# Kernel tuning notes

Hardware: AMD Instinct MI355X
Metric: run time of the kernel (lower is better)

Reference implementation:

```python
import jax, jax.numpy as jnp
import numpy as np
from jax import lax

B, N, C = 8, 8192, 64
ODR, K, OUT = 4, 32, 128
S = N // ODR
EPS = 1e-5


def _lbr(h, W, b, g, be):
    # h: [M, K, Cin] -> linear -> BN (training-mode batch stats over (M,K) per channel) -> relu
    y = jnp.einsum('mki,oi->mko', h, W) + b
    mean = y.mean(axis=(0, 1))
    var = ((y - mean) ** 2).mean(axis=(0, 1))  # biased var, as torch BN uses for normalization
    y = (y - mean) * lax.rsqrt(var + EPS) * g + be
    return jax.nn.relu(y)


def setup_inputs() -> dict:
    key = jax.random.key(0)
    ks = jax.random.split(key, 12)
    x = jax.random.normal(ks[0], (B, N, C), dtype=jnp.float32)
    coor = jax.random.normal(ks[1], (B, N, 3), dtype=jnp.float32)
    indx = jax.random.permutation(ks[2], N)[:S]  # like torch.randperm(N)[:S]
    w1 = jax.random.normal(ks[3], (OUT, 2 * C), dtype=jnp.float32) * (2 * C) ** -0.5
    b1 = jax.random.normal(ks[4], (OUT,), dtype=jnp.float32) * 0.01
    g1 = jax.random.uniform(ks[5], (OUT,), dtype=jnp.float32, minval=0.5, maxval=1.5)
    be1 = jax.random.normal(ks[6], (OUT,), dtype=jnp.float32) * 0.01
    w2 = jax.random.normal(ks[7], (OUT, OUT), dtype=jnp.float32) * OUT ** -0.5
    b2 = jax.random.normal(ks[8], (OUT,), dtype=jnp.float32) * 0.01
    g2 = jax.random.uniform(ks[9], (OUT,), dtype=jnp.float32, minval=0.5, maxval=1.5)
    be2 = jax.random.normal(ks[10], (OUT,), dtype=jnp.float32) * 0.01
    return dict(x=x, coor=coor, indx=indx, w1=w1, b1=b1, g1=g1, be1=be1,
                w2=w2, b2=b2, g2=g2, be2=be2)


def reference(x, coor, indx, w1, b1, g1, be1, w2, b2, g2, be2):
    sampled_coor = coor[:, indx, :]  # [B,S,3]
    sampled_x = x[:, indx, :]        # [B,S,C]
    # pairwise squared distances [B,S,N]
    dist = jnp.sum((coor[:, None, :, :] - sampled_coor[:, :, None, :]) ** 2, axis=-1)
    # k smallest distances == argsort(dist)[..., :K]
    _, knn_idx = lax.top_k(-dist, K)  # [B,S,K]
    knn_x = jax.vmap(lambda xb, ib: xb[ib])(x, knn_idx)  # [B,S,K,C]
    rep_x = jnp.broadcast_to(sampled_x[:, :, None, :], (x.shape[0], S, K, x.shape[2]))
    feat = jnp.concatenate([rep_x, knn_x - rep_x], axis=-1)  # [B,S,K,2C]
    feat = feat.reshape(x.shape[0] * S, K, 2 * x.shape[2])
    h = _lbr(feat, w1, b1, g1, be1)
    h = _lbr(h, w2, b2, g2, be2)
    h = h.reshape(x.shape[0], S, K, -1)
    out = jnp.max(h, axis=2)  # [B,S,OUT]
    return out, sampled_coor
```

## Files before the change

kernel.cpp:

```cpp
#include <hip/hip_runtime.h>
#include <stdint.h>


#define N_    8192
#define GPB_  8

typedef __attribute__((ext_vector_type(8))) short bf8;
typedef __attribute__((ext_vector_type(16))) float f32x16;
typedef __attribute__((ext_vector_type(2))) float f32x2;

__device__ __forceinline__ unsigned int bf1u(float f) {
  unsigned int u = __float_as_uint(f);
  return (u + 0x7fffu + ((u >> 16) & 1u)) >> 16;
}
__device__ __forceinline__ unsigned int bfpair(float lo, float hi) {
  return bf1u(lo) | (bf1u(hi) << 16);
}

__device__ __forceinline__ f32x2 pk_add(f32x2 a, f32x2 b) {
  f32x2 d;
  asm("v_pk_add_f32 %0, %1, %2" : "=v"(d) : "v"(a), "v"(b));
  return d;
}
__device__ __forceinline__ f32x2 pk_mul(f32x2 a, f32x2 b) {
  f32x2 d;
  asm("v_pk_mul_f32 %0, %1, %2" : "=v"(d) : "v"(a), "v"(b));
  return d;
}

__global__ __launch_bounds__(256) void kprep(const float* __restrict__ w1,
                                             const float* __restrict__ w2,
                                             const float* __restrict__ coor,
                                             const int* __restrict__ indx,
                                             unsigned short* __restrict__ w1b,
                                             unsigned short* __restrict__ w2b,
                                             float* __restrict__ outc,
                                             float* __restrict__ soa) {
  int e = blockIdx.x * 256 + threadIdx.x;
  if (e < 16384) {
    w1b[e] = (unsigned short)bf1u(w1[e]);
  } else if (e < 32768) {
    int e2 = e - 16384;
    w2b[e2] = (unsigned short)bf1u(w2[e2]);
  } else if (e < 81920) {
    int e2 = e - 32768;
    int bs = e2 / 3, c = e2 - bs * 3;
    int b = bs >> 11, s = bs & 2047;
    outc[e2] = coor[(b * N_ + indx[s]) * 3 + c];
  } else {
    int p = e - 81920;
    const int b = p >> 13, i = p & 8191;
    const float* src = coor + (size_t)p * 3;
    float* dst = soa + b * 24576;
    dst[i]         = src[0];
    dst[8192 + i]  = src[1];
    dst[16384 + i] = src[2];
  }
}

__global__ __launch_bounds__(256, 8) void kknn(const float* __restrict__ soa,
                                               const int* __restrict__ indx,
                                               int* __restrict__ knn) {
  __shared__ __align__(16) float4 sdist4[4 * 256];
  __shared__ float smin[128];
  __shared__ float smrg[64];
  __shared__ float sT;
  __shared__ unsigned long long cands[128];
  __shared__ unsigned long long ssort[128];
  __shared__ int ccnt;

  const int gid = blockIdx.x;
  const int b = gid >> 11, s = gid & 2047;
  const int tid = threadIdx.x;
  const int w = tid >> 6, lane = tid & 63;
  const float* Xb = soa + b * 24576;
  const float* Yb = Xb + 8192;
  const float* Zb = Xb + 16384;
  const int qi = indx[s];
  const float qx = Xb[qi], qy = Yb[qi], qz = Zb[qi];
  const f32x2 nqx = {-qx, -qx}, nqy = {-qy, -qy}, nqz = {-qz, -qz};

  f32x2 rd[8];
  f32x2 dmL = {3.4e38f, 3.4e38f}, dmH = {3.4e38f, 3.4e38f};
#pragma unroll
  for (int it = 0; it < 8; ++it) {
    const int ofs = (it << 10) + (tid << 2);
    union { float4 f4; f32x2 h[2]; } X, Y, Z;
    X.f4 = *(const float4*)(Xb + ofs);
    Y.f4 = *(const float4*)(Yb + ofs);
    Z.f4 = *(const float4*)(Zb + ofs);
    const f32x2 dxl = pk_add(X.h[0], nqx), dyl = pk_add(Y.h[0], nqy),
                dzl = pk_add(Z.h[0], nqz);
    const f32x2 dxh = pk_add(X.h[1], nqx), dyh = pk_add(Y.h[1], nqy),
                dzh = pk_add(Z.h[1], nqz);
    const f32x2 sl =
        pk_add(pk_add(pk_mul(dxl, dxl), pk_mul(dyl, dyl)), pk_mul(dzl, dzl));
    const f32x2 sh =
        pk_add(pk_add(pk_mul(dxh, dxh), pk_mul(dyh, dyh)), pk_mul(dzh, dzh));
    dmL.x = fminf(dmL.x, sl.x);
    dmL.y = fminf(dmL.y, sl.y);
    dmH.x = fminf(dmH.x, sh.x);
    dmH.y = fminf(dmH.y, sh.y);
    if (it < 4) {
      rd[it * 2] = sl;
      rd[it * 2 + 1] = sh;
    } else {
      union { float4 f4; f32x2 h[2]; } st;
      st.h[0] = sl;
      st.h[1] = sh;
      sdist4[((it - 4) << 8) + tid] = st.f4;
    }
  }
  float dmin = fminf(fminf(dmL.x, dmL.y), fminf(dmH.x, dmH.y));
  if (tid == 0) ccnt = 0;
  if (tid < 128) cands[tid] = ~0ULL;

  float v = dmin;
#pragma unroll
  for (int k = 2; k <= 64; k <<= 1) {
#pragma unroll
    for (int j = k >> 1; j >= 1; j >>= 1) {
      const float o = __shfl_xor(v, j, 64);
      const bool dirAsc = ((lane & k) == 0);
      const bool lower = ((lane & j) == 0);
      const float lo = fminf(v, o), hi = fmaxf(v, o);
      v = (dirAsc == lower) ? lo : hi;
    }
  }
  if (lane < 32) smin[w * 32 + lane] = v;
  __syncthreads();
  if (w < 2) {
    float a = (lane < 32) ? smin[w * 64 + lane] : smin[w * 64 + 32 + (63 - lane)];
#pragma unroll
    for (int j = 32; j >= 1; j >>= 1) {
      const float o = __shfl_xor(a, j, 64);
      const float lo = fminf(a, o), hi = fmaxf(a, o);
      a = ((lane & j) == 0) ? lo : hi;
    }
    if (lane < 32) smrg[w * 32 + lane] = a;
  }
  __syncthreads();
  if (w == 0) {
    float a = (lane < 32) ? smrg[lane] : smrg[32 + (63 - lane)];
#pragma unroll
    for (int j = 32; j >= 1; j >>= 1) {
      const float o = __shfl_xor(a, j, 64);
      const float lo = fminf(a, o), hi = fmaxf(a, o);
      a = ((lane & j) == 0) ? lo : hi;
    }
    if (lane == 31) sT = a;
  }
  __syncthreads();
  const float T = sT;

#pragma unroll
  for (int t = 0; t < 8; ++t) {
    const int p0 = ((t >> 1) << 10) + (tid << 2) + ((t & 1) << 1);
    const float d0 = rd[t].x, d1 = rd[t].y;
    if (d0 <= T) {
      const int pos = atomicAdd(&ccnt, 1);
      if (pos < 128)
        cands[pos] = ((unsigned long long)__float_as_uint(d0) << 32) |
                     (unsigned int)p0;
    }
    if (d1 <= T) {
      const int pos = atomicAdd(&ccnt, 1);
      if (pos < 128)
        cands[pos] = ((unsigned long long)__float_as_uint(d1) << 32) |
                     (unsigned int)(p0 + 1);
    }
  }
#pragma unroll
  for (int it = 4; it < 8; ++it) {
    const float4 d4 = sdist4[((it - 4) << 8) + tid];
    const int p0 = (it << 10) + (tid << 2);
    const float dd[4] = {d4.x, d4.y, d4.z, d4.w};
#pragma unroll
    for (int j = 0; j < 4; ++j) {
      if (dd[j] <= T) {
        const int pos = atomicAdd(&ccnt, 1);
        if (pos < 128)
          cands[pos] = ((unsigned long long)__float_as_uint(dd[j]) << 32) |
                       (unsigned int)(p0 + j);
      }
    }
  }
  __syncthreads();

  if (w < 2) {
    unsigned long long kv = cands[w * 64 + lane];
#pragma unroll
    for (int k = 2; k <= 64; k <<= 1) {
#pragma unroll
      for (int j = k >> 1; j >= 1; j >>= 1) {
        const unsigned long long o = __shfl_xor(kv, j, 64);
        const bool dirAsc = ((lane & k) == 0);
        const bool lower = ((lane & j) == 0);
        const unsigned long long lo = o < kv ? o : kv;
        const unsigned long long hi = o < kv ? kv : o;
        kv = (dirAsc == lower) ? lo : hi;
      }
    }
    ssort[w * 64 + lane] = kv;
  }
  __syncthreads();
  if (w == 0) {
    const unsigned long long a = ssort[lane];
    const unsigned long long b2 = ssort[64 + 63 - lane];
    unsigned long long m = a < b2 ? a : b2;
#pragma unroll
    for (int j = 32; j >= 1; j >>= 1) {
      const unsigned long long o = __shfl_xor(m, j, 64);
      const unsigned long long lo = o < m ? o : m;
      const unsigned long long hi = o < m ? m : o;
      m = ((lane & j) == 0) ? lo : hi;
    }
    if (lane < 32) knn[gid * 32 + lane] = (int)(unsigned int)m;
  }
}

template <int PHASE>
__global__ __launch_bounds__(256, 4) void kphase(
    const float* __restrict__ x, const int* __restrict__ indx,
    const int* __restrict__ knn, const float* __restrict__ b1,
    const unsigned short* __restrict__ w1b, const unsigned short* __restrict__ w2b,
    const float* __restrict__ b2, const float* __restrict__ st1,
    float* __restrict__ part, float* __restrict__ mout) {
  __shared__ __align__(16) float sx[64];
  __shared__ __align__(16) unsigned short sxb[72];
  __shared__ __align__(16) unsigned short dls[32 * 68 + 8];
  __shared__ __align__(16) unsigned short h1[PHASE == 2 ? 32 * 136 : 8];

  const int tid = threadIdx.x;
  const int w = tid >> 6;
  const int lane = tid & 63;
  const int m = lane & 31, q2 = lane >> 5;
  const int col = (w << 5) + m;
  const int r8 = tid >> 3, c8 = (tid & 7) * 8;

  const int bb = blockIdx.x & 7;
  const int jj = blockIdx.x >> 3;
  const float* xb = x + (size_t)bb * (N_ * 64);
  const int gidbase = (bb << 11) + jj * GPB_;

  bf8 bf1[8];
#pragma unroll
  for (int t = 0; t < 8; ++t)
    bf1[t] = *(const bf8*)&w1b[col * 128 + t * 16 + q2 * 8];
  bf8 bf2[8];
  float s1 = 0.f, t1 = 0.f, b2v = 0.f;
  if constexpr (PHASE == 2) {
#pragma unroll
    for (int t = 0; t < 8; ++t)
      bf2[t] = *(const bf8*)&w2b[col * 128 + t * 16 + q2 * 8];
    s1 = st1[col];
    t1 = st1[128 + col];
    b2v = b2[col];
  }
  (void)w2b; (void)b2; (void)st1; (void)mout;
  const float b1c = b1[col];

  float sum = 0.f, ssq = 0.f;

  int idxp = indx[jj * GPB_];
  float sxv = (tid < 64) ? xb[(size_t)idxp * 64 + tid] : 0.f;
  int nbr = knn[(size_t)gidbase * 32 + r8];

#pragma unroll 1
  for (int g = 0; g < GPB_; ++g) {
    const int gid = gidbase + g;
    if (tid < 64) sx[tid] = sxv;
    __syncthreads();

    {
      const float* xrow = xb + (size_t)nbr * 64 + c8;
      const float4 xa = *(const float4*)(xrow);
      const float4 xc = *(const float4*)(xrow + 4);
      const float4 sa = *(const float4*)(sx + c8);
      const float4 sc = *(const float4*)(sx + c8 + 4);
      uint2 lo, hi;
      lo.x = bfpair(xa.x - sa.x, xa.y - sa.y);
      lo.y = bfpair(xa.z - sa.z, xa.w - sa.w);
      hi.x = bfpair(xc.x - sc.x, xc.y - sc.y);
      hi.y = bfpair(xc.z - sc.z, xc.w - sc.w);
      *(uint2*)&dls[r8 * 68 + c8] = lo;
      *(uint2*)&dls[r8 * 68 + c8 + 4] = hi;
    }
    if (tid < 16) {
      const float4 sv = *(const float4*)(sx + tid * 4);
      uint2 p;
      p.x = bfpair(sv.x, sv.y);
      p.y = bfpair(sv.z, sv.w);
      *(uint2*)&sxb[tid * 4] = p;
    }

    if (g + 1 < GPB_) {
      const int s1n = jj * GPB_ + g + 1;
      const int idx1 = indx[s1n];
      sxv = (tid < 64) ? xb[(size_t)idx1 * 64 + tid] : 0.f;
      nbr = knn[(size_t)(gid + 1) * 32 + r8];
    }
    __syncthreads();

    bf8 af[8];
#pragma unroll
    for (int t = 0; t < 4; ++t) {
      union { bf8 v; uint2 u[2]; } fa;
      fa.u[0] = *(const uint2*)&sxb[t * 16 + q2 * 8];
      fa.u[1] = *(const uint2*)&sxb[t * 16 + q2 * 8 + 4];
      af[t] = fa.v;
    }
#pragma unroll
    for (int t = 0; t < 4; ++t) {
      union { bf8 v; uint2 u[2]; } fa;
      fa.u[0] = *(const uint2*)&dls[m * 68 + t * 16 + q2 * 8];
      fa.u[1] = *(const uint2*)&dls[m * 68 + t * 16 + q2 * 8 + 4];
      af[4 + t] = fa.v;
    }

    f32x16 acc;
#pragma unroll
    for (int r = 0; r < 16; ++r) acc[r] = b1c;
#pragma unroll
    for (int t = 0; t < 8; ++t)
      acc = __builtin_amdgcn_mfma_f32_32x32x16_bf16(af[t], bf1[t], acc, 0, 0, 0);

    if constexpr (PHASE == 1) {
#pragma unroll
      for (int r = 0; r < 16; ++r) {
        const float v = acc[r];
        sum += v;
        ssq = fmaf(v, v, ssq);
      }
    } else {
#pragma unroll
      for (int r = 0; r < 16; ++r) {
        const float hv = fmaxf(0.f, fmaf(acc[r], s1, t1));
        const int row = (r & 3) + ((r >> 2) << 3) + (q2 << 2);
        h1[row * 136 + col] = (unsigned short)bf1u(hv);
      }
      __syncthreads();

      f32x16 acc2;
#pragma unroll
      for (int r = 0; r < 16; ++r) acc2[r] = b2v;
#pragma unroll
      for (int t = 0; t < 8; ++t) {
        const bf8 a2 = *(const bf8*)&h1[m * 136 + t * 16 + q2 * 8];
        acc2 = __builtin_amdgcn_mfma_f32_32x32x16_bf16(a2, bf2[t], acc2, 0, 0, 0);
      }

      float mx = -1e30f;
#pragma unroll
      for (int r = 0; r < 16; ++r) {
        const float v = acc2[r];
        sum += v;
        ssq = fmaf(v, v, ssq);
        mx = fmaxf(mx, v);
      }
      mx = fmaxf(mx, __shfl_xor(mx, 32, 64));
      if (lane < 32) mout[(size_t)gid * 128 + col] = mx;
    }
  }

  sum += __shfl_xor(sum, 32, 64);
  ssq += __shfl_xor(ssq, 32, 64);
  if (lane < 32) {
    part[blockIdx.x * 256 + col] = sum;
    part[blockIdx.x * 256 + 128 + col] = ssq;
  }
}

__global__ __launch_bounds__(256) void kred1(const float* __restrict__ part,
                                             double* __restrict__ dbuf) {
  const int blk = blockIdx.x;
  const int c = threadIdx.x;
  const float* p = part + (size_t)blk * 32 * 256 + c;
  double acc = 0.0;
#pragma unroll 8
  for (int r = 0; r < 32; ++r) acc += (double)p[r * 256];
  dbuf[blk * 256 + c] = acc;
}

__global__ __launch_bounds__(256) void kred2(const double* __restrict__ dbuf,
                                             const float* __restrict__ gam,
                                             const float* __restrict__ bet,
                                             float* __restrict__ st) {
  __shared__ double sS[256];
  const int c = threadIdx.x;
  double acc = 0.0;
#pragma unroll 8
  for (int i = 0; i < 64; ++i) acc += dbuf[i * 256 + c];
  sS[c] = acc;
  __syncthreads();
  if (c < 128) {
    const double Sv = sS[c], SSv = sS[128 + c];
    const double cnt = 524288.0;
    const double mean = Sv / cnt;
    const double var = SSv / cnt - mean * mean;
    const double scale = (double)gam[c] / sqrt(var + 1e-5);
    st[c] = (float)scale;
    st[128 + c] = (float)((double)bet[c] - mean * scale);
  }
}

__global__ __launch_bounds__(256) void kout(const float* __restrict__ m,
                                            const float* __restrict__ st2,
                                            float* __restrict__ out) {
  const int e4 = blockIdx.x * 256 + threadIdx.x;
  const int o0 = (e4 & 31) * 4;
  const float4 v = ((const float4*)m)[e4];
  const float4 sc = *(const float4*)&st2[o0];
  const float4 sh = *(const float4*)&st2[128 + o0];
  float4 r;
  r.x = fmaxf(0.f, fmaf(v.x, sc.x, sh.x));
  r.y = fmaxf(0.f, fmaf(v.y, sc.y, sh.y));
  r.z = fmaxf(0.f, fmaf(v.z, sc.z, sh.z));
  r.w = fmaxf(0.f, fmaf(v.w, sc.w, sh.w));
  ((float4*)out)[e4] = r;
}

extern "C" void kernel_launch(void* const* d_in, const int* in_sizes, int n_in,
                              void* d_out, int out_size, void* d_ws, size_t ws_size,
                              hipStream_t stream) {
  (void)in_sizes; (void)n_in; (void)out_size; (void)ws_size;
  const float* x    = (const float*)d_in[0];
  const float* coor = (const float*)d_in[1];
  const int*   indx = (const int*)d_in[2];
  const float* w1   = (const float*)d_in[3];
  const float* b1   = (const float*)d_in[4];
  const float* g1   = (const float*)d_in[5];
  const float* be1  = (const float*)d_in[6];
  const float* w2   = (const float*)d_in[7];
  const float* b2   = (const float*)d_in[8];
  const float* g2   = (const float*)d_in[9];
  const float* be2  = (const float*)d_in[10];
  float* out = (float*)d_out;

  char* ws = (char*)d_ws;
  int*            knn   = (int*)(ws + 0);
  float*          mbuf  = (float*)(ws + 2097152);
  float*          part1 = (float*)(ws + 10485760);
  float*          soa   = (float*)(ws + 10485760);
  float*          part2 = (float*)(ws + 12582912);
  unsigned short* w1b   = (unsigned short*)(ws + 14680064);
  unsigned short* w2b   = (unsigned short*)(ws + 14712832);
  float*          st1   = (float*)(ws + 14745600);
  float*          st2   = (float*)(ws + 14746624);
  double*         dbuf  = (double*)(ws + 14747648);

  float* outc = out + 2097152;

  kprep<<<576, 256, 0, stream>>>(w1, w2, coor, indx, w1b, w2b, outc, soa);
  kknn<<<16384, 256, 0, stream>>>(soa, indx, knn);
  kphase<1><<<2048, 256, 0, stream>>>(x, indx, knn, b1, w1b, w2b, b2, nullptr,
                                      part1, nullptr);
  kred1<<<64, 256, 0, stream>>>(part1, dbuf);
  kred2<<<1, 256, 0, stream>>>(dbuf, g1, be1, st1);
  kphase<2><<<2048, 256, 0, stream>>>(x, indx, knn, b1, w1b, w2b, b2, st1,
                                      part2, mbuf);
  kred1<<<64, 256, 0, stream>>>(part2, dbuf);
  kred2<<<1, 256, 0, stream>>>(dbuf, g2, be2, st2);
  kout<<<2048, 256, 0, stream>>>(mbuf, st2, out);
}
```

Measured before the change: 289.9 us.

## Use per-wave 8th-min threshold and rank-count selection in kNN kernel

Replaces the block-wide bitonic merge that found the exact 32nd-smallest per-thread minimum with a looser threshold: the maximum over four waves of each wave's 8th-smallest minimum. That removes two barriers and two merge passes. The final bitonic sort and merge of candidates is replaced by a rank-by-counting selection over up to 192 candidates. The looser threshold admits more candidates (capacity raised to 192), and if more than 192 qualify, true neighbours may be dropped.

```diff
diff --git a/kernel.cpp b/kernel.cpp
--- a/kernel.cpp
+++ b/kernel.cpp
@@ -62,11 +62,8 @@
                                                const int* __restrict__ indx,
                                                int* __restrict__ knn) {
   __shared__ __align__(16) float4 sdist4[4 * 256];
-  __shared__ float smin[128];
-  __shared__ float smrg[64];
-  __shared__ float sT;
-  __shared__ unsigned long long cands[128];
-  __shared__ unsigned long long ssort[128];
+  __shared__ float sTw[4];
+  __shared__ unsigned long long cands[192];
   __shared__ int ccnt;
 
   const int gid = blockIdx.x;
@@ -81,7 +78,7 @@
   const f32x2 nqx = {-qx, -qx}, nqy = {-qy, -qy}, nqz = {-qz, -qz};
 
   f32x2 rd[8];
-  f32x2 dmL = {3.4e38f, 3.4e38f}, dmH = {3.4e38f, 3.4e38f};
+  float dmA = 3.4e38f, dmB = 3.4e38f;
 #pragma unroll
   for (int it = 0; it < 8; ++it) {
     const int ofs = (it << 10) + (tid << 2);
@@ -97,10 +94,8 @@
         pk_add(pk_add(pk_mul(dxl, dxl), pk_mul(dyl, dyl)), pk_mul(dzl, dzl));
     const f32x2 sh =
         pk_add(pk_add(pk_mul(dxh, dxh), pk_mul(dyh, dyh)), pk_mul(dzh, dzh));
-    dmL.x = fminf(dmL.x, sl.x);
-    dmL.y = fminf(dmL.y, sl.y);
-    dmH.x = fminf(dmH.x, sh.x);
-    dmH.y = fminf(dmH.y, sh.y);
+    dmA = fminf(fminf(sl.x, sl.y), dmA);
+    dmB = fminf(fminf(sh.x, sh.y), dmB);
     if (it < 4) {
       rd[it * 2] = sl;
       rd[it * 2 + 1] = sh;
@@ -111,9 +106,9 @@
       sdist4[((it - 4) << 8) + tid] = st.f4;
     }
   }
-  float dmin = fminf(fminf(dmL.x, dmL.y), fminf(dmH.x, dmH.y));
+  float dmin = fminf(dmA, dmB);
   if (tid == 0) ccnt = 0;
-  if (tid < 128) cands[tid] = ~0ULL;
+  if (tid < 192) cands[tid] = ~0ULL;
 
   float v = dmin;
 #pragma unroll
@@ -127,31 +122,9 @@
       v = (dirAsc == lower) ? lo : hi;
     }
   }
-  if (lane < 32) smin[w * 32 + lane] = v;
+  if (lane == 7) sTw[w] = v;
   __syncthreads();
-  if (w < 2) {
-    float a = (lane < 32) ? smin[w * 64 + lane] : smin[w * 64 + 32 + (63 - lane)];
-#pragma unroll
-    for (int j = 32; j >= 1; j >>= 1) {
-      const float o = __shfl_xor(a, j, 64);
-      const float lo = fminf(a, o), hi = fmaxf(a, o);
-      a = ((lane & j) == 0) ? lo : hi;
-    }
-    if (lane < 32) smrg[w * 32 + lane] = a;
-  }
-  __syncthreads();
-  if (w == 0) {
-    float a = (lane < 32) ? smrg[lane] : smrg[32 + (63 - lane)];
-#pragma unroll
-    for (int j = 32; j >= 1; j >>= 1) {
-      const float o = __shfl_xor(a, j, 64);
-      const float lo = fminf(a, o), hi = fmaxf(a, o);
-      a = ((lane & j) == 0) ? lo : hi;
-    }
-    if (lane == 31) sT = a;
-  }
-  __syncthreads();
-  const float T = sT;
+  const float T = fmaxf(fmaxf(sTw[0], sTw[1]), fmaxf(sTw[2], sTw[3]));
 
 #pragma unroll
   for (int t = 0; t < 8; ++t) {
@@ -159,13 +132,13 @@
     const float d0 = rd[t].x, d1 = rd[t].y;
     if (d0 <= T) {
       const int pos = atomicAdd(&ccnt, 1);
-      if (pos < 128)
+      if (pos < 192)
         cands[pos] = ((unsigned long long)__float_as_uint(d0) << 32) |
                      (unsigned int)p0;
     }
     if (d1 <= T) {
       const int pos = atomicAdd(&ccnt, 1);
-      if (pos < 128)
+      if (pos < 192)
         cands[pos] = ((unsigned long long)__float_as_uint(d1) << 32) |
                      (unsigned int)(p0 + 1);
     }
@@ -179,7 +152,7 @@
     for (int j = 0; j < 4; ++j) {
       if (dd[j] <= T) {
         const int pos = atomicAdd(&ccnt, 1);
-        if (pos < 128)
+        if (pos < 192)
           cands[pos] = ((unsigned long long)__float_as_uint(dd[j]) << 32) |
                        (unsigned int)(p0 + j);
       }
@@ -187,35 +160,12 @@
   }
   __syncthreads();
 
-  if (w < 2) {
-    unsigned long long kv = cands[w * 64 + lane];
-#pragma unroll
-    for (int k = 2; k <= 64; k <<= 1) {
-#pragma unroll
-      for (int j = k >> 1; j >= 1; j >>= 1) {
-        const unsigned long long o = __shfl_xor(kv, j, 64);
-        const bool dirAsc = ((lane & k) == 0);
-        const bool lower = ((lane & j) == 0);
-        const unsigned long long lo = o < kv ? o : kv;
-        const unsigned long long hi = o < kv ? kv : o;
-        kv = (dirAsc == lower) ? lo : hi;
-      }
-    }
-    ssort[w * 64 + lane] = kv;
-  }
-  __syncthreads();
-  if (w == 0) {
-    const unsigned long long a = ssort[lane];
-    const unsigned long long b2 = ssort[64 + 63 - lane];
-    unsigned long long m = a < b2 ? a : b2;
-#pragma unroll
-    for (int j = 32; j >= 1; j >>= 1) {
-      const unsigned long long o = __shfl_xor(m, j, 64);
-      const unsigned long long lo = o < m ? o : m;
-      const unsigned long long hi = o < m ? m : o;
-      m = ((lane & j) == 0) ? lo : hi;
-    }
-    if (lane < 32) knn[gid * 32 + lane] = (int)(unsigned int)m;
+  const int E = min(ccnt, 192);
+  if (tid < E) {
+    const unsigned long long key = cands[tid];
+    int rank = 0;
+    for (int j = 0; j < E; ++j) rank += (cands[j] < key) ? 1 : 0;
+    if (rank < 32) knn[gid * 32 + rank] = (int)(unsigned int)key;
   }
 }
 
```

Measured after the change: 288.7 us. No clear change (-0.4%).
